# Optimization experiments

Hardware: AMD Instinct MI355X
Metric: run time of the kernel (lower is better)

The kernel has to match this reference:

```python
import jax, jax.numpy as jnp
import numpy as np

HID = 1024
SEQ = 8192


def setup_inputs() -> dict:
    key = jax.random.key(0)
    ks = jax.random.split(key, 7)
    s = 1.0 / np.sqrt(HID)  # PyTorch LSTM/Linear default init scale
    return {
        "sentence": jax.random.normal(ks[0], (SEQ,), dtype=jnp.float32),
        "W_ih": jax.random.normal(ks[1], (4 * HID, 1), dtype=jnp.float32) * s,
        "W_hh": jax.random.normal(ks[2], (4 * HID, HID), dtype=jnp.float32) * s,
        "b_ih": jax.random.normal(ks[3], (4 * HID,), dtype=jnp.float32) * s,
        "b_hh": jax.random.normal(ks[4], (4 * HID,), dtype=jnp.float32) * s,
        "W_lin": jax.random.normal(ks[5], (1, HID), dtype=jnp.float32) * s,
        "b_lin": jax.random.normal(ks[6], (1,), dtype=jnp.float32) * s,
    }


def reference(sentence, W_ih, W_hh, b_ih, b_hh, W_lin, b_lin):
    H = W_hh.shape[1]
    b = b_ih + b_hh  # fold the two biases once, outside the scan

    def step(carry, x):
        h, c = carry  # each [H]
        # gate pre-activations: [4H]. input_size=1 so W_ih @ x is a scaled column.
        z = W_ih[:, 0] * x + W_hh @ h + b
        i = jax.nn.sigmoid(z[0 * H:1 * H])
        f = jax.nn.sigmoid(z[1 * H:2 * H])
        g = jnp.tanh(z[2 * H:3 * H])
        o = jax.nn.sigmoid(z[3 * H:4 * H])
        c_new = f * c + i * g
        h_new = o * jnp.tanh(c_new)
        out = W_lin @ h_new + b_lin  # [1], the per-timestep Linear(hidden)
        return (h_new, c_new), out

    h0 = jnp.zeros((H,), dtype=sentence.dtype)
    c0 = jnp.zeros((H,), dtype=sentence.dtype)
    _, outputs = jax.lax.scan(step, (h0, c0), sentence)
    return outputs  # [SEQ, 1], the stacked list of outputs
```

## Files before the change

kernel.cpp:

```cpp
#include <hip/hip_runtime.h>


#define SEQ 8192
#define HID 1024
#define NWG 128
#define TPB 512
#define NWAVE 8

typedef unsigned long long ull;

__device__ __forceinline__ float fast_sigmoid(float z) {
    float e = __builtin_amdgcn_exp2f(-1.4426950408889634f * z);
    return 1.0f / (1.0f + e);
}
__device__ __forceinline__ float fast_tanh(float x) {
    float e = __builtin_amdgcn_exp2f(2.8853900817779268f * x);
    return 1.0f - 2.0f / (e + 1.0f);
}

__global__ void init_kernel(float* out, const float* __restrict__ b_lin) {
    int i = blockIdx.x * blockDim.x + threadIdx.x;
    if (i < SEQ) out[i] = b_lin[0];
}

__global__ void finish_kernel(const float* __restrict__ partials,
                              float* __restrict__ out) {
    int t = blockIdx.x * blockDim.x + threadIdx.x;
    if (t >= SEQ) return;
    float s = out[t];
    #pragma unroll 4
    for (int g2 = 0; g2 < NWG; ++g2) s += partials[(size_t)g2 * SEQ + t];
    out[t] = s;
}

__global__ __launch_bounds__(TPB, 2)
void lstm_kernel(const float* __restrict__ sentence,
                 const float* __restrict__ W_ih,
                 const float* __restrict__ W_hh,
                 const float* __restrict__ b_ih,
                 const float* __restrict__ b_hh,
                 const float* __restrict__ W_lin,
                 ull* slots, float* partials, float* out, int use_partials)
{
    __shared__ float s_sent[SEQ];
    __shared__ float s_h[HID];
    __shared__ float s_part[2][NWAVE];
    const int tid = threadIdx.x;
    const int g = blockIdx.x;
    const int w = tid >> 6;
    const int l = tid & 63;
    const int j = g * NWAVE + w;

    for (int i = tid; i < SEQ; i += TPB) s_sent[i] = sentence[i];

    float Wa[4][16];
    #pragma unroll
    for (int gate = 0; gate < 4; ++gate) {
        const float* rowp = W_hh + (size_t)(j + gate * HID) * HID;
        #pragma unroll
        for (int k = 0; k < 16; ++k) {
            float tmp = rowp[k * 64 + l];
            asm volatile("v_accvgpr_write_b32 %0, %1" : "=a"(Wa[gate][k]) : "v"(tmp));
        }
    }
    float wih[4], bb[4];
    #pragma unroll
    for (int gate = 0; gate < 4; ++gate) {
        int row = j + gate * HID;
        wih[gate] = W_ih[row];
        bb[gate]  = b_ih[row] + b_hh[row];
    }
    const float wlin = W_lin[j];
    float c = 0.0f;

    ull* const buf0 = slots;
    ull* const buf1 = slots + HID;

    __syncthreads();

    for (int t = 0; t < SEQ; ++t) {
        if (t == 0) {
            s_h[tid] = 0.0f;
            s_h[tid + TPB] = 0.0f;
        } else {
            ull* b = (t & 1) ? buf1 : buf0;
            const unsigned tt = (unsigned)t;
            float h0 = 0.0f, h1 = 0.0f;
            bool d0 = false, d1 = false;
            int guard = 0;
            for (;;) {
                if (!d0) {
                    ull v = __hip_atomic_load(&b[tid], __ATOMIC_RELAXED, __HIP_MEMORY_SCOPE_AGENT);
                    if ((unsigned)(v >> 32) == tt) { h0 = __uint_as_float((unsigned)v); d0 = true; }
                }
                if (!d1) {
                    ull v = __hip_atomic_load(&b[tid + TPB], __ATOMIC_RELAXED, __HIP_MEMORY_SCOPE_AGENT);
                    if ((unsigned)(v >> 32) == tt) { h1 = __uint_as_float((unsigned)v); d1 = true; }
                }
                if (d0 && d1) break;
                if (++guard > (1 << 24)) break;
            }
            s_h[tid]       = h0;
            s_h[tid + TPB] = h1;
        }
        __syncthreads();

        if (t > 0 && tid == 0) {
            const float* sp = s_part[(t - 1) & 1];
            float p = sp[0] + sp[1] + sp[2] + sp[3] + sp[4] + sp[5] + sp[6] + sp[7];
            if (use_partials) partials[(size_t)g * SEQ + (t - 1)] = p;
            else atomicAdd(&out[t - 1], p);
        }

        float acc0 = 0.f, acc1 = 0.f, acc2 = 0.f, acc3 = 0.f;
        #pragma unroll
        for (int k = 0; k < 16; ++k) {
            const float hk = s_h[k * 64 + l];
            float w0, w1, w2, w3;
            asm volatile("v_accvgpr_read_b32 %0, %1" : "=v"(w0) : "a"(Wa[0][k]));
            asm volatile("v_accvgpr_read_b32 %0, %1" : "=v"(w1) : "a"(Wa[1][k]));
            asm volatile("v_accvgpr_read_b32 %0, %1" : "=v"(w2) : "a"(Wa[2][k]));
            asm volatile("v_accvgpr_read_b32 %0, %1" : "=v"(w3) : "a"(Wa[3][k]));
            acc0 = fmaf(w0, hk, acc0);
            acc1 = fmaf(w1, hk, acc1);
            acc2 = fmaf(w2, hk, acc2);
            acc3 = fmaf(w3, hk, acc3);
        }
        #pragma unroll
        for (int m = 1; m < 64; m <<= 1) {
            acc0 += __shfl_xor(acc0, m, 64);
            acc1 += __shfl_xor(acc1, m, 64);
            acc2 += __shfl_xor(acc2, m, 64);
            acc3 += __shfl_xor(acc3, m, 64);
        }

        const float x = s_sent[t];
        float zi = fmaf(wih[0], x, acc0 + bb[0]);
        float zf = fmaf(wih[1], x, acc1 + bb[1]);
        float zg = fmaf(wih[2], x, acc2 + bb[2]);
        float zo = fmaf(wih[3], x, acc3 + bb[3]);
        c = fmaf(fast_sigmoid(zf), c, fast_sigmoid(zi) * fast_tanh(zg));
        const float hn = fast_sigmoid(zo) * fast_tanh(c);

        if (l == 0) {
            ull pk = ((ull)(unsigned)(t + 1) << 32) | (ull)__float_as_uint(hn);
            __hip_atomic_store(&(((t + 1) & 1) ? buf1 : buf0)[j], pk,
                               __ATOMIC_RELAXED, __HIP_MEMORY_SCOPE_AGENT);
            s_part[t & 1][w] = wlin * hn;
        }
    }

    __syncthreads();
    if (tid == 0) {
        const float* sp = s_part[(SEQ - 1) & 1];
        float p = sp[0] + sp[1] + sp[2] + sp[3] + sp[4] + sp[5] + sp[6] + sp[7];
        if (use_partials) partials[(size_t)g * SEQ + (SEQ - 1)] = p;
        else atomicAdd(&out[SEQ - 1], p);
    }
}

extern "C" void kernel_launch(void* const* d_in, const int* in_sizes, int n_in,
                              void* d_out, int out_size, void* d_ws, size_t ws_size,
                              hipStream_t stream) {
    const float* sentence = (const float*)d_in[0];
    const float* W_ih     = (const float*)d_in[1];
    const float* W_hh     = (const float*)d_in[2];
    const float* b_ih     = (const float*)d_in[3];
    const float* b_hh     = (const float*)d_in[4];
    const float* W_lin    = (const float*)d_in[5];
    const float* b_lin    = (const float*)d_in[6];
    float* out = (float*)d_out;

    char* ws = (char*)d_ws;
    ull* slots      = (ull*)ws;
    float* partials = (float*)(ws + 2 * HID * sizeof(ull));
    const size_t need = 2 * HID * sizeof(ull) + (size_t)NWG * SEQ * sizeof(float);
    int use_partials = (ws_size >= need) ? 1 : 0;

    hipLaunchKernelGGL(init_kernel, dim3(SEQ / 256), dim3(256), 0, stream,
                       out, b_lin);
    hipLaunchKernelGGL(lstm_kernel, dim3(NWG), dim3(TPB), 0, stream,
                       sentence, W_ih, W_hh, b_ih, b_hh, W_lin,
                       slots, partials, out, use_partials);
    if (use_partials) {
        hipLaunchKernelGGL(finish_kernel, dim3(SEQ / 256), dim3(256), 0, stream,
                           partials, out);
    }
}
```

Measured before the change: 31.08 ms.

## Split LSTM workgroup into compute, loader and output waves with chunked h-ready flags

Each workgroup gains extra waves. One dedicated loader wave polls the global h slots and publishes chunks into double-buffered shared memory with a per-chunk ready bitmask. The compute waves start their dot products per chunk as soon as that chunk is ready, instead of waiting on a full __syncthreads. Workgroup 0 also gets a wave that computes the Linear output directly from the full h vector, which removes the init and finish kernels and the per-group partial sums. The risks are added polling contention on shared memory and correctness that relies on the ordering of the workgroup-scope acquire and release flags.

```diff
diff --git a/kernel.cpp b/kernel.cpp
--- a/kernel.cpp
+++ b/kernel.cpp
@@ -4,8 +4,8 @@
 #define SEQ 8192
 #define HID 1024
 #define NWG 128
-#define TPB 512
-#define NWAVE 8
+#define TPB 640
+#define NCW 8
 
 typedef unsigned long long ull;
 
@@ -18,21 +18,6 @@
     return 1.0f - 2.0f / (e + 1.0f);
 }
 
-__global__ void init_kernel(float* out, const float* __restrict__ b_lin) {
-    int i = blockIdx.x * blockDim.x + threadIdx.x;
-    if (i < SEQ) out[i] = b_lin[0];
-}
-
-__global__ void finish_kernel(const float* __restrict__ partials,
-                              float* __restrict__ out) {
-    int t = blockIdx.x * blockDim.x + threadIdx.x;
-    if (t >= SEQ) return;
-    float s = out[t];
-    #pragma unroll 4
-    for (int g2 = 0; g2 < NWG; ++g2) s += partials[(size_t)g2 * SEQ + t];
-    out[t] = s;
-}
-
 __global__ __launch_bounds__(TPB, 2)
 void lstm_kernel(const float* __restrict__ sentence,
                  const float* __restrict__ W_ih,
@@ -40,122 +25,151 @@
                  const float* __restrict__ b_ih,
                  const float* __restrict__ b_hh,
                  const float* __restrict__ W_lin,
-                 ull* slots, float* partials, float* out, int use_partials)
+                 const float* __restrict__ b_lin,
+                 ull* slots, float* out)
 {
     __shared__ float s_sent[SEQ];
-    __shared__ float s_h[HID];
-    __shared__ float s_part[2][NWAVE];
+    __shared__ float s_h[2][HID];
+    __shared__ unsigned s_mask[2];
     const int tid = threadIdx.x;
     const int g = blockIdx.x;
     const int w = tid >> 6;
     const int l = tid & 63;
-    const int j = g * NWAVE + w;
 
     for (int i = tid; i < SEQ; i += TPB) s_sent[i] = sentence[i];
+    if (tid < 2) s_mask[tid] = 0u;
+    for (int i = tid; i < 2 * HID; i += TPB) ((float*)s_h)[i] = 0.0f;
 
     float Wa[4][16];
-    #pragma unroll
-    for (int gate = 0; gate < 4; ++gate) {
-        const float* rowp = W_hh + (size_t)(j + gate * HID) * HID;
+    float wih[4], bb[4];
+    float wl[16];
+    float blin = 0.0f;
+    float wdummy = 0.0f;
+    if (w < NCW) {
+        const int j = g * NCW + w;
         #pragma unroll
-        for (int k = 0; k < 16; ++k) {
-            float tmp = rowp[k * 64 + l];
-            asm volatile("v_accvgpr_write_b32 %0, %1" : "=a"(Wa[gate][k]) : "v"(tmp));
+        for (int gate = 0; gate < 4; ++gate) {
+            const float* rowp = W_hh + (size_t)(j + gate * HID) * HID;
+            #pragma unroll
+            for (int k = 0; k < 16; ++k) {
+                float tmp = rowp[k * 64 + l];
+                asm volatile("v_accvgpr_write_b32 %0, %1" : "=a"(Wa[gate][k]) : "v"(tmp));
+            }
         }
+        #pragma unroll
+        for (int gate = 0; gate < 4; ++gate) {
+            int row = j + gate * HID;
+            wih[gate] = W_ih[row];
+            bb[gate]  = b_ih[row] + b_hh[row];
+        }
+    } else if (w == NCW + 1) {
+        #pragma unroll
+        for (int k = 0; k < 16; ++k) wl[k] = W_lin[k * 64 + l];
+        blin = b_lin[0];
     }
-    float wih[4], bb[4];
-    #pragma unroll
-    for (int gate = 0; gate < 4; ++gate) {
-        int row = j + gate * HID;
-        wih[gate] = W_ih[row];
-        bb[gate]  = b_ih[row] + b_hh[row];
-    }
-    const float wlin = W_lin[j];
-    float c = 0.0f;
-
-    ull* const buf0 = slots;
-    ull* const buf1 = slots + HID;
-
+    (void)wdummy;
     __syncthreads();
 
-    for (int t = 0; t < SEQ; ++t) {
-        if (t == 0) {
-            s_h[tid] = 0.0f;
-            s_h[tid + TPB] = 0.0f;
-        } else {
-            ull* b = (t & 1) ? buf1 : buf0;
+    if (w < NCW) {
+        const int j = g * NCW + w;
+        float c = 0.0f;
+        for (int t = 0; t < SEQ; ++t) {
+            const int p = t & 1;
+            float a0 = 0.f, a1 = 0.f, a2 = 0.f, a3 = 0.f;
+            if (t > 0) {
+                const unsigned tt = (unsigned)t;
+                unsigned have = 0u;
+                int guard = 0;
+                #pragma unroll
+                for (int k = 0; k < 16; ++k) {
+                    while (!((have >> k) & 1u)) {
+                        unsigned mv = __hip_atomic_load(&s_mask[p], __ATOMIC_ACQUIRE,
+                                                        __HIP_MEMORY_SCOPE_WORKGROUP);
+                        have = ((mv >> 16) == tt) ? (mv & 0xFFFFu) : 0u;
+                        if (++guard > (1 << 22)) have = 0xFFFFu;
+                    }
+                    const float hk = s_h[p][k * 64 + l];
+                    float w0, w1, w2, w3;
+                    asm volatile("v_accvgpr_read_b32 %0, %1" : "=v"(w0) : "a"(Wa[0][k]));
+                    asm volatile("v_accvgpr_read_b32 %0, %1" : "=v"(w1) : "a"(Wa[1][k]));
+                    asm volatile("v_accvgpr_read_b32 %0, %1" : "=v"(w2) : "a"(Wa[2][k]));
+                    asm volatile("v_accvgpr_read_b32 %0, %1" : "=v"(w3) : "a"(Wa[3][k]));
+                    a0 = fmaf(w0, hk, a0);
+                    a1 = fmaf(w1, hk, a1);
+                    a2 = fmaf(w2, hk, a2);
+                    a3 = fmaf(w3, hk, a3);
+                }
+            }
+            #pragma unroll
+            for (int m = 1; m < 64; m <<= 1) {
+                a0 += __shfl_xor(a0, m, 64);
+                a1 += __shfl_xor(a1, m, 64);
+                a2 += __shfl_xor(a2, m, 64);
+                a3 += __shfl_xor(a3, m, 64);
+            }
+            const float x = s_sent[t];
+            float zi = fmaf(wih[0], x, a0 + bb[0]);
+            float zf = fmaf(wih[1], x, a1 + bb[1]);
+            float zg = fmaf(wih[2], x, a2 + bb[2]);
+            float zo = fmaf(wih[3], x, a3 + bb[3]);
+            c = fmaf(fast_sigmoid(zf), c, fast_sigmoid(zi) * fast_tanh(zg));
+            const float hn = fast_sigmoid(zo) * fast_tanh(c);
+            if (l == 0) {
+                ull pk = ((ull)(unsigned)(t + 1) << 32) | (ull)__float_as_uint(hn);
+                __hip_atomic_store(&slots[(size_t)(((t + 1) & 1)) * HID + j], pk,
+                                   __ATOMIC_RELAXED, __HIP_MEMORY_SCOPE_AGENT);
+                asm volatile("" ::: "memory");
+            }
+        }
+    } else if (w == NCW) {
+        for (int t = 1; t <= SEQ; ++t) {
+            const int p = t & 1;
             const unsigned tt = (unsigned)t;
-            float h0 = 0.0f, h1 = 0.0f;
-            bool d0 = false, d1 = false;
+            ull* bg = slots + (size_t)p * HID;
+            unsigned pend = 0xFFFFu, mask = 0u;
             int guard = 0;
-            for (;;) {
-                if (!d0) {
-                    ull v = __hip_atomic_load(&b[tid], __ATOMIC_RELAXED, __HIP_MEMORY_SCOPE_AGENT);
-                    if ((unsigned)(v >> 32) == tt) { h0 = __uint_as_float((unsigned)v); d0 = true; }
+            while (pend) {
+                ull v[16];
+                #pragma unroll
+                for (int k = 0; k < 16; ++k)
+                    if ((pend >> k) & 1u)
+                        v[k] = __hip_atomic_load(&bg[k * 64 + l], __ATOMIC_RELAXED,
+                                                 __HIP_MEMORY_SCOPE_AGENT);
+                unsigned newly = 0u;
+                #pragma unroll
+                for (int k = 0; k < 16; ++k)
+                    if ((pend >> k) & 1u)
+                        if (__all((int)((unsigned)(v[k] >> 32) == tt)))
+                            newly |= (1u << k);
+                if (newly) {
+                    #pragma unroll
+                    for (int k = 0; k < 16; ++k)
+                        if ((newly >> k) & 1u)
+                            s_h[p][k * 64 + l] = __uint_as_float((unsigned)v[k]);
+                    mask |= newly;
+                    pend &= ~newly;
+                    if (l == 0)
+                        __hip_atomic_store(&s_mask[p], (tt << 16) | mask,
+                                           __ATOMIC_RELEASE, __HIP_MEMORY_SCOPE_WORKGROUP);
                 }
-                if (!d1) {
-                    ull v = __hip_atomic_load(&b[tid + TPB], __ATOMIC_RELAXED, __HIP_MEMORY_SCOPE_AGENT);
-                    if ((unsigned)(v >> 32) == tt) { h1 = __uint_as_float((unsigned)v); d1 = true; }
-                }
-                if (d0 && d1) break;
+                if (++guard > (1 << 20)) break;
+            }
+        }
+    } else if (g == 0) {
+        for (int t = 1; t <= SEQ; ++t) {
+            const int p = t & 1;
+            const unsigned want = ((unsigned)t << 16) | 0xFFFFu;
+            int guard = 0;
+            while (__hip_atomic_load(&s_mask[p], __ATOMIC_ACQUIRE,
+                                     __HIP_MEMORY_SCOPE_WORKGROUP) != want)
                 if (++guard > (1 << 24)) break;
-            }
-            s_h[tid]       = h0;
-            s_h[tid + TPB] = h1;
+            float po = 0.f;
+            #pragma unroll
+            for (int k = 0; k < 16; ++k) po = fmaf(wl[k], s_h[p][k * 64 + l], po);
+            #pragma unroll
+            for (int m = 1; m < 64; m <<= 1) po += __shfl_xor(po, m, 64);
+            if (l == 0) out[t - 1] = po + blin;
         }
-        __syncthreads();
-
-        if (t > 0 && tid == 0) {
-            const float* sp = s_part[(t - 1) & 1];
-            float p = sp[0] + sp[1] + sp[2] + sp[3] + sp[4] + sp[5] + sp[6] + sp[7];
-            if (use_partials) partials[(size_t)g * SEQ + (t - 1)] = p;
-            else atomicAdd(&out[t - 1], p);
-        }
-
-        float acc0 = 0.f, acc1 = 0.f, acc2 = 0.f, acc3 = 0.f;
-        #pragma unroll
-        for (int k = 0; k < 16; ++k) {
-            const float hk = s_h[k * 64 + l];
-            float w0, w1, w2, w3;
-            asm volatile("v_accvgpr_read_b32 %0, %1" : "=v"(w0) : "a"(Wa[0][k]));
-            asm volatile("v_accvgpr_read_b32 %0, %1" : "=v"(w1) : "a"(Wa[1][k]));
-            asm volatile("v_accvgpr_read_b32 %0, %1" : "=v"(w2) : "a"(Wa[2][k]));
-            asm volatile("v_accvgpr_read_b32 %0, %1" : "=v"(w3) : "a"(Wa[3][k]));
-            acc0 = fmaf(w0, hk, acc0);
-            acc1 = fmaf(w1, hk, acc1);
-            acc2 = fmaf(w2, hk, acc2);
-            acc3 = fmaf(w3, hk, acc3);
-        }
-        #pragma unroll
-        for (int m = 1; m < 64; m <<= 1) {
-            acc0 += __shfl_xor(acc0, m, 64);
-            acc1 += __shfl_xor(acc1, m, 64);
-            acc2 += __shfl_xor(acc2, m, 64);
-            acc3 += __shfl_xor(acc3, m, 64);
-        }
-
-        const float x = s_sent[t];
-        float zi = fmaf(wih[0], x, acc0 + bb[0]);
-        float zf = fmaf(wih[1], x, acc1 + bb[1]);
-        float zg = fmaf(wih[2], x, acc2 + bb[2]);
-        float zo = fmaf(wih[3], x, acc3 + bb[3]);
-        c = fmaf(fast_sigmoid(zf), c, fast_sigmoid(zi) * fast_tanh(zg));
-        const float hn = fast_sigmoid(zo) * fast_tanh(c);
-
-        if (l == 0) {
-            ull pk = ((ull)(unsigned)(t + 1) << 32) | (ull)__float_as_uint(hn);
-            __hip_atomic_store(&(((t + 1) & 1) ? buf1 : buf0)[j], pk,
-                               __ATOMIC_RELAXED, __HIP_MEMORY_SCOPE_AGENT);
-            s_part[t & 1][w] = wlin * hn;
-        }
-    }
-
-    __syncthreads();
-    if (tid == 0) {
-        const float* sp = s_part[(SEQ - 1) & 1];
-        float p = sp[0] + sp[1] + sp[2] + sp[3] + sp[4] + sp[5] + sp[6] + sp[7];
-        if (use_partials) partials[(size_t)g * SEQ + (SEQ - 1)] = p;
-        else atomicAdd(&out[SEQ - 1], p);
     }
 }
 
@@ -171,19 +185,9 @@
     const float* b_lin    = (const float*)d_in[6];
     float* out = (float*)d_out;
 
-    char* ws = (char*)d_ws;
-    ull* slots      = (ull*)ws;
-    float* partials = (float*)(ws + 2 * HID * sizeof(ull));
-    const size_t need = 2 * HID * sizeof(ull) + (size_t)NWG * SEQ * sizeof(float);
-    int use_partials = (ws_size >= need) ? 1 : 0;
+    ull* slots = (ull*)d_ws;
 
-    hipLaunchKernelGGL(init_kernel, dim3(SEQ / 256), dim3(256), 0, stream,
-                       out, b_lin);
     hipLaunchKernelGGL(lstm_kernel, dim3(NWG), dim3(TPB), 0, stream,
-                       sentence, W_ih, W_hh, b_ih, b_hh, W_lin,
-                       slots, partials, out, use_partials);
-    if (use_partials) {
-        hipLaunchKernelGGL(finish_kernel, dim3(SEQ / 256), dim3(256), 0, stream,
-                           partials, out);
-    }
+                       sentence, W_ih, W_hh, b_ih, b_hh, W_lin, b_lin,
+                       slots, out);
 }
```

New measurement: 38.46 ms. +23.7%, slower.
